# Performance work log

Hardware: AMD Instinct MI355X
Metric: run time of the kernel (lower is better)

Reference implementation:

```python
import jax, jax.numpy as jnp
import numpy as np

NODE_FEAT_DIM = 140
CONFIG_FEAT_DIM = 24
N_OPS = 120
OP_EMB_DIM = 8
H_DIM = 64
N_LAYERS = 3
N_NODES = 5000
N_EDGES = 8000
N_CONFIGS = 32
IN_DIM = NODE_FEAT_DIM + OP_EMB_DIM + CONFIG_FEAT_DIM  # 172


def setup_inputs() -> dict:
    key = jax.random.key(0)
    ks = jax.random.split(key, 24)
    s = 0.05
    inp = {
        'node_feat': jax.random.normal(ks[0], (1, N_NODES, NODE_FEAT_DIM), jnp.float32),
        'node_opcode': jax.random.randint(ks[1], (1, N_NODES), 0, N_OPS, jnp.int64),
        'edge_index': jax.random.randint(ks[2], (1, N_EDGES, 2), 0, N_NODES, jnp.int64),
        'config_feat': jax.random.normal(ks[3], (1, N_CONFIGS, CONFIG_FEAT_DIM), jnp.float32),
        'op_emb': jax.random.normal(ks[4], (N_OPS, OP_EMB_DIM), jnp.float32) * s,
        # layer 0 SAGE weights (in_dim=172), layers 1..2 stacked (h->h)
        'w_self0': jax.random.normal(ks[5], (IN_DIM, H_DIM), jnp.float32) * s,
        'w_neigh0': jax.random.normal(ks[6], (IN_DIM, H_DIM), jnp.float32) * s,
        'b0': jnp.zeros((H_DIM,), jnp.float32),
        'w_self': jax.random.normal(ks[7], (N_LAYERS - 1, H_DIM, H_DIM), jnp.float32) * s,
        'w_neigh': jax.random.normal(ks[8], (N_LAYERS - 1, H_DIM, H_DIM), jnp.float32) * s,
        'b': jnp.zeros((N_LAYERS - 1, H_DIM), jnp.float32),
        'skip_w': jax.random.normal(ks[9], (N_LAYERS, H_DIM, H_DIM), jnp.float32) * s,
        'skip_b': jnp.zeros((N_LAYERS, H_DIM), jnp.float32),
        'p1_w': jax.random.normal(ks[10], (N_LAYERS * H_DIM, (N_LAYERS - 1) * H_DIM), jnp.float32) * s,
        'p1_b': jnp.zeros(((N_LAYERS - 1) * H_DIM,), jnp.float32),
        'p2_w': jax.random.normal(ks[11], ((N_LAYERS - 1) * H_DIM, H_DIM), jnp.float32) * s,
        'p2_b': jnp.zeros((H_DIM,), jnp.float32),
        'p3_w': jax.random.normal(ks[12], (H_DIM, 1), jnp.float32) * s,
        'p3_b': jnp.zeros((1,), jnp.float32),
    }
    return inp


def _sage(x, src, dst, w_self, w_neigh, bias):
    # x: (N, C, D); bidirectional mean aggregation over edges, then linear + ReLU
    n = x.shape[0]
    msg = jax.ops.segment_sum(x[src], dst, num_segments=n)          # (N, C, D)
    deg = jax.ops.segment_sum(jnp.ones(src.shape, x.dtype), dst, num_segments=n)
    agg = msg / jnp.maximum(deg, 1.0)[:, None, None]
    return jax.nn.relu(jnp.einsum('ncd,dh->nch', x, w_self)
                       + jnp.einsum('ncd,dh->nch', agg, w_neigh) + bias)


def reference(node_feat, node_opcode, edge_index, config_feat,
              op_emb, w_self0, w_neigh0, b0, w_self, w_neigh, b,
              skip_w, skip_b, p1_w, p1_b, p2_w, p2_b, p3_w, p3_b):
    nf = node_feat[0]                     # (N, 140)
    op = node_opcode[0]                   # (N,)
    ei = edge_index[0]                    # (M, 2)
    cf = config_feat[0]                   # (C, 24)
    n_nodes, n_configs = nf.shape[0], cf.shape[0]

    # early join: node feats + op embedding broadcast with config feats
    xn = jnp.concatenate([nf, op_emb[op]], axis=-1)                     # (N, 148)
    x = jnp.concatenate([
        jnp.broadcast_to(xn[:, None, :], (n_nodes, n_configs, xn.shape[-1])),
        jnp.broadcast_to(cf[None, :, :], (n_nodes, n_configs, cf.shape[-1])),
    ], axis=-1)                                                          # (N, C, 172)

    # bidirectional edge list
    src = jnp.concatenate([ei[:, 0], ei[:, 1]])
    dst = jnp.concatenate([ei[:, 1], ei[:, 0]])

    skips = []
    x = _sage(x, src, dst, w_self0, w_neigh0, b0)
    skips.append(jax.nn.relu(jnp.einsum('nch,hk->nck', x, skip_w[0]) + skip_b[0]))
    for l in range(N_LAYERS - 1):
        x = _sage(x, src, dst, w_self[l], w_neigh[l], b[l])
        skips.append(jax.nn.relu(jnp.einsum('nch,hk->nck', x, skip_w[l + 1]) + skip_b[l + 1]))

    x = jnp.concatenate(skips, axis=-1)          # (N, C, 3*H)
    x = x.sum(axis=0)                            # global_add_pool over nodes -> (C, 3*H)
    x = jax.nn.relu(x @ p1_w + p1_b)
    x = jax.nn.relu(x @ p2_w + p2_b)
    return (x @ p3_w + p3_b)[:, 0]               # (C,)
```

## Files before the change

### kernel.cpp

```cpp
#include <hip/hip_runtime.h>

#define N_NODESC 5000
#define N_EDGESC 8000
#define NCFG 32
#define HDIM 64
#define NF_DIM 140
#define OPE_DIM 8
#define XN_DIM 148
#define CF_DIM 24
#define NBLK_SAGE 512
#define NW_SAGE (NBLK_SAGE * 4)
#define NBLK_H0 512
#define NW_H0 (NBLK_H0 * 4)

using f32x4 = __attribute__((ext_vector_type(4))) float;
using bf16x8 = __attribute__((ext_vector_type(8))) short;

__device__ __forceinline__ ushort f2b(float f) {
    uint u = __float_as_uint(f);
    u += 0x7FFF + ((u >> 16) & 1);
    return (ushort)(u >> 16);
}
__device__ __forceinline__ float b2f(ushort u) {
    return __uint_as_float(((uint)u) << 16);
}

__global__ void k_deg(const int* __restrict__ ei, int* __restrict__ deg) {
    int t = blockIdx.x * blockDim.x + threadIdx.x;
    if (t >= 2 * N_EDGESC) return;
    int d;
    if (t < N_EDGESC) d = ei[2 * t + 1];
    else d = ei[2 * (t - N_EDGESC)];
    atomicAdd(&deg[d], 1);
}

__global__ void k_scan(const int* __restrict__ deg, int* __restrict__ row_ptr) {
    __shared__ int ssum[1024];
    int t = threadIdx.x;
    const int per = (N_NODESC + 1023) / 1024;
    int vals[8];
    int loc = 0;
    for (int i = 0; i < per; ++i) {
        int idx = t * per + i;
        int v = (idx < N_NODESC) ? deg[idx] : 0;
        vals[i] = loc;
        loc += v;
    }
    ssum[t] = loc;
    __syncthreads();
    for (int s = 1; s < 1024; s <<= 1) {
        int v = (t >= s) ? ssum[t - s] : 0;
        __syncthreads();
        ssum[t] += v;
        __syncthreads();
    }
    int excl = ssum[t] - loc;
    for (int i = 0; i < per; ++i) {
        int idx = t * per + i;
        if (idx < N_NODESC) row_ptr[idx] = excl + vals[i];
    }
    if (t == 1023) row_ptr[N_NODESC] = ssum[1023];
}

__global__ void k_fill(const int* __restrict__ ei, const int* __restrict__ row_ptr,
                       int* __restrict__ fill, int* __restrict__ col) {
    int t = blockIdx.x * blockDim.x + threadIdx.x;
    if (t >= 2 * N_EDGESC) return;
    int s, d;
    if (t < N_EDGESC) { s = ei[2 * t]; d = ei[2 * t + 1]; }
    else { int e = t - N_EDGESC; s = ei[2 * e + 1]; d = ei[2 * e]; }
    int pos = atomicAdd(&fill[d], 1);
    col[row_ptr[d] + pos] = s;
}

__global__ __launch_bounds__(512) void k_pack(const float* __restrict__ skw,
                                              const float* __restrict__ wsl,
                                              const float* __restrict__ wnl,
                                              ushort* __restrict__ frag) {
    int m = blockIdx.x;
    const float* W;
    switch (m) {
        case 0: W = skw; break;
        case 1: W = wsl; break;
        case 2: W = wnl; break;
        case 3: W = skw + 4096; break;
        case 4: W = wsl + 4096; break;
        case 5: W = wnl + 4096; break;
        default: W = skw + 8192; break;
    }
    int t = threadIdx.x;
    int ktnt = t >> 6, lane = t & 63;
    int kt = ktnt >> 2, nt = ktnt & 3;
    int g = lane >> 4, row16 = lane & 15;
    bf16x8 v;
#pragma unroll
    for (int j = 0; j < 8; ++j)
        v[j] = (short)f2b(W[(kt * 32 + g * 8 + j) * HDIM + nt * 16 + row16]);
    *reinterpret_cast<bf16x8*>(frag + (size_t)m * 4096 + (size_t)t * 8) = v;
}

__global__ void k_xn(const float* __restrict__ nf, const int* __restrict__ opcode,
                     const float* __restrict__ op_emb, float* __restrict__ xn) {
    int t = blockIdx.x * blockDim.x + threadIdx.x;
    if (t >= N_NODESC * XN_DIM) return;
    int n = t / XN_DIM, f = t - n * XN_DIM;
    float v;
    if (f < NF_DIM) v = nf[n * NF_DIM + f];
    else v = op_emb[opcode[n] * OPE_DIM + (f - NF_DIM)];
    xn[t] = v;
}

__global__ void k_aggn(const float* __restrict__ xn, const int* __restrict__ row_ptr,
                       const int* __restrict__ col, float* __restrict__ aggn) {
    int t = blockIdx.x * blockDim.x + threadIdx.x;
    if (t >= N_NODESC * XN_DIM) return;
    int n = t / XN_DIM, f = t - n * XN_DIM;
    int rs = row_ptr[n], re = row_ptr[n + 1];
    float s = 0.f;
    for (int j = rs; j < re; ++j) s += xn[col[j] * XN_DIM + f];
    float inv = (re > rs) ? 1.0f / (float)(re - rs) : 0.f;
    aggn[t] = s * inv;
}

__global__ void k_En(const float* __restrict__ xn, const float* __restrict__ aggn,
                     const float* __restrict__ Ws0, const float* __restrict__ Wn0,
                     float* __restrict__ En) {
    int t = blockIdx.x * blockDim.x + threadIdx.x;
    if (t >= N_NODESC * HDIM) return;
    int n = t >> 6, k = t & 63;
    const float* x = xn + n * XN_DIM;
    const float* a = aggn + n * XN_DIM;
    float s = 0.f;
    for (int d = 0; d < XN_DIM; ++d)
        s += x[d] * Ws0[d * HDIM + k] + a[d] * Wn0[d * HDIM + k];
    En[t] = s;
}

__global__ void k_cf(const float* __restrict__ cf, const float* __restrict__ Ws0,
                     const float* __restrict__ Wn0, const float* __restrict__ b0,
                     float* __restrict__ Fc, float* __restrict__ Gc) {
    int t = threadIdx.x;
    for (int i = t; i < NCFG * HDIM; i += 256) {
        int c = i >> 6, k = i & 63;
        float f = b0[k], g = 0.f;
        for (int d = 0; d < CF_DIM; ++d) {
            float v = cf[c * CF_DIM + d];
            f += v * Ws0[(XN_DIM + d) * HDIM + k];
            g += v * Wn0[(XN_DIM + d) * HDIM + k];
        }
        Fc[i] = f;
        Gc[i] = g;
    }
}

__global__ __launch_bounds__(256) void k_h0skip(
    const float* __restrict__ En, const float* __restrict__ Fc,
    const float* __restrict__ Gc, const int* __restrict__ deg,
    const ushort* __restrict__ fragSk, const float* __restrict__ skB,
    ushort* __restrict__ h0, float* __restrict__ partials) {
    __shared__ float sred[4][NCFG * HDIM];
    int lane = threadIdx.x & 63;
    int row16 = lane & 15, g = lane >> 4;
    int w = threadIdx.x >> 6;
    int gw = (blockIdx.x * 256 + threadIdx.x) >> 6;

    bf16x8 bSk[2][4];
#pragma unroll
    for (int kt = 0; kt < 2; ++kt)
#pragma unroll
        for (int nt = 0; nt < 4; ++nt)
            bSk[kt][nt] = *reinterpret_cast<const bf16x8*>(
                fragSk + ((kt * 4 + nt) * 64 + lane) * 8);
    float sb[4];
#pragma unroll
    for (int nt = 0; nt < 4; ++nt) sb[nt] = skB[nt * 16 + row16];

    float fcv[2][2][8], gcv[2][2][8];
#pragma unroll
    for (int mt = 0; mt < 2; ++mt)
#pragma unroll
        for (int kt = 0; kt < 2; ++kt) {
            int base = (row16 + 16 * mt) * HDIM + kt * 32 + g * 8;
            float4 f0 = *(const float4*)&Fc[base];
            float4 f1 = *(const float4*)&Fc[base + 4];
            float4 g0 = *(const float4*)&Gc[base];
            float4 g1 = *(const float4*)&Gc[base + 4];
            fcv[mt][kt][0] = f0.x; fcv[mt][kt][1] = f0.y; fcv[mt][kt][2] = f0.z; fcv[mt][kt][3] = f0.w;
            fcv[mt][kt][4] = f1.x; fcv[mt][kt][5] = f1.y; fcv[mt][kt][6] = f1.z; fcv[mt][kt][7] = f1.w;
            gcv[mt][kt][0] = g0.x; gcv[mt][kt][1] = g0.y; gcv[mt][kt][2] = g0.z; gcv[mt][kt][3] = g0.w;
            gcv[mt][kt][4] = g1.x; gcv[mt][kt][5] = g1.y; gcv[mt][kt][6] = g1.z; gcv[mt][kt][7] = g1.w;
        }

    f32x4 skipAcc[2][4];
#pragma unroll
    for (int mt = 0; mt < 2; ++mt)
#pragma unroll
        for (int nt = 0; nt < 4; ++nt) skipAcc[mt][nt] = f32x4{0.f, 0.f, 0.f, 0.f};

    for (int n = gw; n < N_NODESC; n += NW_H0) {
        float sc = (deg[n] > 0) ? 1.f : 0.f;
        const float* enp = En + (size_t)n * HDIM;
        float en[2][8];
#pragma unroll
        for (int kt = 0; kt < 2; ++kt) {
            float4 e0 = *(const float4*)&enp[kt * 32 + g * 8];
            float4 e1 = *(const float4*)&enp[kt * 32 + g * 8 + 4];
            en[kt][0] = e0.x; en[kt][1] = e0.y; en[kt][2] = e0.z; en[kt][3] = e0.w;
            en[kt][4] = e1.x; en[kt][5] = e1.y; en[kt][6] = e1.z; en[kt][7] = e1.w;
        }
        bf16x8 aH[2][2];
#pragma unroll
        for (int mt = 0; mt < 2; ++mt)
#pragma unroll
            for (int kt = 0; kt < 2; ++kt) {
                bf16x8 a;
#pragma unroll
                for (int j = 0; j < 8; ++j) {
                    float hv = fmaxf(en[kt][j] + fcv[mt][kt][j] + sc * gcv[mt][kt][j], 0.f);
                    a[j] = (short)f2b(hv);
                }
                aH[mt][kt] = a;
                *reinterpret_cast<bf16x8*>(
                    h0 + (size_t)n * (NCFG * HDIM) + (row16 + 16 * mt) * HDIM + kt * 32 + g * 8) = a;
            }
#pragma unroll
        for (int mt = 0; mt < 2; ++mt)
#pragma unroll
            for (int nt = 0; nt < 4; ++nt) {
                f32x4 c2 = f32x4{0.f, 0.f, 0.f, 0.f};
#pragma unroll
                for (int kt = 0; kt < 2; ++kt)
                    c2 = __builtin_amdgcn_mfma_f32_16x16x32_bf16(aH[mt][kt], bSk[kt][nt], c2, 0, 0, 0);
#pragma unroll
                for (int r = 0; r < 4; ++r)
                    skipAcc[mt][nt][r] += fmaxf(c2[r] + sb[nt], 0.f);
            }
    }

#pragma unroll
    for (int mt = 0; mt < 2; ++mt)
#pragma unroll
        for (int nt = 0; nt < 4; ++nt)
#pragma unroll
            for (int r = 0; r < 4; ++r)
                sred[w][(16 * mt + 4 * g + r) * HDIM + 16 * nt + row16] = skipAcc[mt][nt][r];
    __syncthreads();
    float* pb = partials + (size_t)blockIdx.x * (NCFG * HDIM);
#pragma unroll
    for (int q = 0; q < 2; ++q) {
        int p = threadIdx.x * 8 + q * 4;
        f32x4 s = *(const f32x4*)&sred[0][p];
        s += *(const f32x4*)&sred[1][p];
        s += *(const f32x4*)&sred[2][p];
        s += *(const f32x4*)&sred[3][p];
        *(f32x4*)&pb[p] = s;
    }
}

template <int STORE_H>
__global__ __launch_bounds__(256) void k_sage_mfma(
    const ushort* __restrict__ h_in, ushort* __restrict__ h_out,
    const ushort* __restrict__ fragWs, const ushort* __restrict__ fragWn,
    const ushort* __restrict__ fragSk,
    const float* __restrict__ bias, const float* __restrict__ skB,
    const int* __restrict__ row_ptr, const int* __restrict__ col,
    float* __restrict__ partials) {
    __shared__ ushort sstage[4][32 * 72];
    __shared__ float sred[4][NCFG * HDIM];
    int lane = threadIdx.x & 63;
    int row16 = lane & 15, g = lane >> 4;
    int w = threadIdx.x >> 6;
    int gw = (blockIdx.x * 256 + threadIdx.x) >> 6;
    ushort* st = sstage[w];

    bf16x8 bWs[2][4], bWn[2][4], bSk[2][4];
#pragma unroll
    for (int kt = 0; kt < 2; ++kt)
#pragma unroll
        for (int nt = 0; nt < 4; ++nt) {
            int fo = ((kt * 4 + nt) * 64 + lane) * 8;
            bWs[kt][nt] = *reinterpret_cast<const bf16x8*>(fragWs + fo);
            bWn[kt][nt] = *reinterpret_cast<const bf16x8*>(fragWn + fo);
            bSk[kt][nt] = *reinterpret_cast<const bf16x8*>(fragSk + fo);
        }
    float bb[4], sb[4];
#pragma unroll
    for (int nt = 0; nt < 4; ++nt) {
        bb[nt] = bias[nt * 16 + row16];
        sb[nt] = skB[nt * 16 + row16];
    }
    f32x4 skipAcc[2][4];
#pragma unroll
    for (int mt = 0; mt < 2; ++mt)
#pragma unroll
        for (int nt = 0; nt < 4; ++nt) skipAcc[mt][nt] = f32x4{0.f, 0.f, 0.f, 0.f};

    int loff[2][2];
#pragma unroll
    for (int mt = 0; mt < 2; ++mt)
#pragma unroll
        for (int kt = 0; kt < 2; ++kt)
            loff[mt][kt] = (row16 + 16 * mt) * HDIM + kt * 32 + g * 8;

    for (int n = gw; n < N_NODESC; n += NW_SAGE) {
        const ushort* hb = h_in + (size_t)n * (NCFG * HDIM);
        bf16x8 aS[2][2];
#pragma unroll
        for (int mt = 0; mt < 2; ++mt)
#pragma unroll
            for (int kt = 0; kt < 2; ++kt)
                aS[mt][kt] = *reinterpret_cast<const bf16x8*>(hb + loff[mt][kt]);

        float agg[2][2][8];
#pragma unroll
        for (int mt = 0; mt < 2; ++mt)
#pragma unroll
            for (int kt = 0; kt < 2; ++kt)
#pragma unroll
                for (int j = 0; j < 8; ++j) agg[mt][kt][j] = 0.f;
        int rs = row_ptr[n], re = row_ptr[n + 1];
        for (int e = rs; e < re; ++e) {
            const ushort* nb = h_in + (size_t)col[e] * (NCFG * HDIM);
#pragma unroll
            for (int mt = 0; mt < 2; ++mt)
#pragma unroll
                for (int kt = 0; kt < 2; ++kt) {
                    bf16x8 u = *reinterpret_cast<const bf16x8*>(nb + loff[mt][kt]);
#pragma unroll
                    for (int j = 0; j < 8; ++j) agg[mt][kt][j] += b2f((ushort)u[j]);
                }
        }
        float inv = (re > rs) ? 1.f / (float)(re - rs) : 0.f;
        bf16x8 aA[2][2];
#pragma unroll
        for (int mt = 0; mt < 2; ++mt)
#pragma unroll
            for (int kt = 0; kt < 2; ++kt)
#pragma unroll
                for (int j = 0; j < 8; ++j)
                    aA[mt][kt][j] = (short)f2b(agg[mt][kt][j] * inv);

        f32x4 C[2][4];
#pragma unroll
        for (int mt = 0; mt < 2; ++mt)
#pragma unroll
            for (int nt = 0; nt < 4; ++nt) {
                f32x4 c = f32x4{0.f, 0.f, 0.f, 0.f};
#pragma unroll
                for (int kt = 0; kt < 2; ++kt) {
                    c = __builtin_amdgcn_mfma_f32_16x16x32_bf16(aS[mt][kt], bWs[kt][nt], c, 0, 0, 0);
                    c = __builtin_amdgcn_mfma_f32_16x16x32_bf16(aA[mt][kt], bWn[kt][nt], c, 0, 0, 0);
                }
                C[mt][nt] = c;
            }

#pragma unroll
        for (int mt = 0; mt < 2; ++mt)
#pragma unroll
            for (int nt = 0; nt < 4; ++nt)
#pragma unroll
                for (int r = 0; r < 4; ++r) {
                    float hv = fmaxf(C[mt][nt][r] + bb[nt], 0.f);
                    st[(16 * mt + 4 * g + r) * 72 + 16 * nt + row16] = f2b(hv);
                }
        asm volatile("s_waitcnt lgkmcnt(0)" ::: "memory");

        if (STORE_H) {
#pragma unroll
            for (int i = 0; i < 4; ++i) {
                int e2 = i * 512 + lane * 8;
                int cc = e2 >> 6, dd = e2 & 63;
                bf16x8 v = *reinterpret_cast<const bf16x8*>(st + cc * 72 + dd);
                *reinterpret_cast<bf16x8*>(h_out + (size_t)n * (NCFG * HDIM) + e2) = v;
            }
        }

        bf16x8 aH[2][2];
#pragma unroll
        for (int mt = 0; mt < 2; ++mt)
#pragma unroll
            for (int kt = 0; kt < 2; ++kt)
                aH[mt][kt] = *reinterpret_cast<const bf16x8*>(
                    st + (row16 + 16 * mt) * 72 + kt * 32 + g * 8);
#pragma unroll
        for (int mt = 0; mt < 2; ++mt)
#pragma unroll
            for (int nt = 0; nt < 4; ++nt) {
                f32x4 c2 = f32x4{0.f, 0.f, 0.f, 0.f};
#pragma unroll
                for (int kt = 0; kt < 2; ++kt)
                    c2 = __builtin_amdgcn_mfma_f32_16x16x32_bf16(aH[mt][kt], bSk[kt][nt], c2, 0, 0, 0);
#pragma unroll
                for (int r = 0; r < 4; ++r)
                    skipAcc[mt][nt][r] += fmaxf(c2[r] + sb[nt], 0.f);
            }
        asm volatile("s_waitcnt lgkmcnt(0)" ::: "memory");
    }

#pragma unroll
    for (int mt = 0; mt < 2; ++mt)
#pragma unroll
        for (int nt = 0; nt < 4; ++nt)
#pragma unroll
            for (int r = 0; r < 4; ++r)
                sred[w][(16 * mt + 4 * g + r) * HDIM + 16 * nt + row16] = skipAcc[mt][nt][r];
    __syncthreads();
    float* pb = partials + (size_t)blockIdx.x * (NCFG * HDIM);
#pragma unroll
    for (int q = 0; q < 2; ++q) {
        int p = threadIdx.x * 8 + q * 4;
        f32x4 s = *(const f32x4*)&sred[0][p];
        s += *(const f32x4*)&sred[1][p];
        s += *(const f32x4*)&sred[2][p];
        s += *(const f32x4*)&sred[3][p];
        *(f32x4*)&pb[p] = s;
    }
}

__global__ __launch_bounds__(256) void k_redA(const float* __restrict__ partials,
                                              int nrows, float* __restrict__ part2) {
    int i = blockIdx.x * 256 + threadIdx.x;
    int jb = blockIdx.y;
    int seg = nrows >> 5;
    const float* p = partials + (size_t)jb * seg * (NCFG * HDIM) + i;
    float s = 0.f;
    for (int b = 0; b < seg; ++b) s += p[(size_t)b * (NCFG * HDIM)];
    part2[jb * (NCFG * HDIM) + i] = s;
}

__global__ __launch_bounds__(256) void k_redB(const float* __restrict__ part2,
                                              float* __restrict__ S, int lcol) {
    int i = blockIdx.x * 256 + threadIdx.x;
    float s = 0.f;
#pragma unroll
    for (int b = 0; b < 32; ++b) s += part2[b * (NCFG * HDIM) + i];
    int c = i >> 6, k = i & 63;
    S[c * (3 * HDIM) + lcol * HDIM + k] = s;
}

__global__ void k_mlp(const float* __restrict__ S,
                      const float* __restrict__ p1w, const float* __restrict__ p1b,
                      const float* __restrict__ p2w, const float* __restrict__ p2b,
                      const float* __restrict__ p3w, const float* __restrict__ p3b,
                      float* __restrict__ out) {
    int c = blockIdx.x;
    int t = threadIdx.x;
    __shared__ float sx[192];
    __shared__ float h1[128];
    __shared__ float h2[64];
    if (t < 192) sx[t] = S[c * 192 + t];
    __syncthreads();
    if (t < 128) {
        float s = p1b[t];
        for (int d = 0; d < 192; ++d) s += sx[d] * p1w[d * 128 + t];
        h1[t] = fmaxf(s, 0.f);
    }
    __syncthreads();
    if (t < 64) {
        float s = p2b[t];
        for (int d = 0; d < 128; ++d) s += h1[d] * p2w[d * 64 + t];
        h2[t] = fmaxf(s, 0.f);
    }
    __syncthreads();
    if (t == 0) {
        float s = p3b[0];
        for (int d = 0; d < 64; ++d) s += h2[d] * p3w[d];
        out[c] = s;
    }
}

extern "C" void kernel_launch(void* const* d_in, const int* in_sizes, int n_in,
                              void* d_out, int out_size, void* d_ws, size_t ws_size,
                              hipStream_t stream) {
    const float* nf  = (const float*)d_in[0];
    const int*   opc = (const int*)d_in[1];
    const int*   ei  = (const int*)d_in[2];
    const float* cf  = (const float*)d_in[3];
    const float* ope = (const float*)d_in[4];
    const float* ws0 = (const float*)d_in[5];
    const float* wn0 = (const float*)d_in[6];
    const float* b0  = (const float*)d_in[7];
    const float* wsl = (const float*)d_in[8];
    const float* wnl = (const float*)d_in[9];
    const float* bl  = (const float*)d_in[10];
    const float* skw = (const float*)d_in[11];
    const float* skb = (const float*)d_in[12];
    const float* p1w = (const float*)d_in[13];
    const float* p1b = (const float*)d_in[14];
    const float* p2w = (const float*)d_in[15];
    const float* p2b = (const float*)d_in[16];
    const float* p3w = (const float*)d_in[17];
    const float* p3b = (const float*)d_in[18];
    float* out = (float*)d_out;

    char* w = (char*)d_ws;
    auto alloc = [&](size_t bytes) {
        char* p = w;
        w += (bytes + 255) & ~(size_t)255;
        return p;
    };
    int* deg      = (int*)alloc(N_NODESC * 4);
    int* row_ptr  = (int*)alloc((N_NODESC + 1) * 4);
    int* fill     = (int*)alloc(N_NODESC * 4);
    int* col      = (int*)alloc(2 * N_EDGESC * 4);
    float* xn     = (float*)alloc((size_t)N_NODESC * XN_DIM * 4);
    float* aggn   = (float*)alloc((size_t)N_NODESC * XN_DIM * 4);
    float* En     = (float*)alloc((size_t)N_NODESC * HDIM * 4);
    float* Fc     = (float*)alloc(NCFG * HDIM * 4);
    float* Gc     = (float*)alloc(NCFG * HDIM * 4);
    float* S      = (float*)alloc(NCFG * 3 * HDIM * 4);
    float* part2  = (float*)alloc(32 * NCFG * HDIM * 4);
    ushort* frag  = (ushort*)alloc(7 * 4096 * 2);
    float* p0     = (float*)alloc((size_t)NBLK_H0 * NCFG * HDIM * 4);
    float* p1     = (float*)alloc((size_t)NBLK_SAGE * NCFG * HDIM * 4);
    float* p2     = (float*)alloc((size_t)NBLK_SAGE * NCFG * HDIM * 4);
    ushort* h0    = (ushort*)alloc((size_t)N_NODESC * NCFG * HDIM * 2);
    ushort* h1    = (ushort*)alloc((size_t)N_NODESC * NCFG * HDIM * 2);

    hipMemsetAsync(deg, 0, N_NODESC * 4, stream);
    hipMemsetAsync(fill, 0, N_NODESC * 4, stream);
    k_deg<<<(2 * N_EDGESC + 255) / 256, 256, 0, stream>>>(ei, deg);
    k_scan<<<1, 1024, 0, stream>>>(deg, row_ptr);
    k_fill<<<(2 * N_EDGESC + 255) / 256, 256, 0, stream>>>(ei, row_ptr, fill, col);
    k_pack<<<7, 512, 0, stream>>>(skw, wsl, wnl, frag);
    k_xn<<<(N_NODESC * XN_DIM + 255) / 256, 256, 0, stream>>>(nf, opc, ope, xn);
    k_aggn<<<(N_NODESC * XN_DIM + 255) / 256, 256, 0, stream>>>(xn, row_ptr, col, aggn);
    k_En<<<(N_NODESC * HDIM + 255) / 256, 256, 0, stream>>>(xn, aggn, ws0, wn0, En);
    k_cf<<<1, 256, 0, stream>>>(cf, ws0, wn0, b0, Fc, Gc);

    k_h0skip<<<NBLK_H0, 256, 0, stream>>>(En, Fc, Gc, deg, frag, skb, h0, p0);
    k_sage_mfma<1><<<NBLK_SAGE, 256, 0, stream>>>(
        h0, h1, frag + 1 * 4096, frag + 2 * 4096, frag + 3 * 4096,
        bl, skb + 64, row_ptr, col, p1);
    k_sage_mfma<0><<<NBLK_SAGE, 256, 0, stream>>>(
        h1, (ushort*)nullptr, frag + 4 * 4096, frag + 5 * 4096, frag + 6 * 4096,
        bl + 64, skb + 2 * 64, row_ptr, col, p2);

    dim3 gA(8, 32);
    k_redA<<<gA, 256, 0, stream>>>(p0, NBLK_H0, part2);
    k_redB<<<8, 256, 0, stream>>>(part2, S, 0);
    k_redA<<<gA, 256, 0, stream>>>(p1, NBLK_SAGE, part2);
    k_redB<<<8, 256, 0, stream>>>(part2, S, 1);
    k_redA<<<gA, 256, 0, stream>>>(p2, NBLK_SAGE, part2);
    k_redB<<<8, 256, 0, stream>>>(part2, S, 2);
    k_mlp<<<NCFG, 256, 0, stream>>>(S, p1w, p1b, p2w, p2b, p3w, p3b, out);
}
```

Measured before the change: 177.9 us.

## Project layer-0 features before aggregation, one node per wave, fewer kernel launches

Layer 0 now multiplies node features by both weight matrices first and aggregates the 64-wide projected neighbour values, instead of aggregating the 148-wide inputs. This cuts aggregation traffic and removes the xn and aggn buffers. The SAGE and h0 kernels switch from a grid-stride loop to one node per wave on 1250 blocks. The per-layer reductions are merged into a single 3D launch with the final stage folded into the MLP, and the config projection is folded into the pack kernel. The partial-sum buffers grow, so the reduction reads more data, and shared memory is aliased between staging and reduction, which needs an extra barrier.

```diff
diff --git a/kernel.cpp b/kernel.cpp
--- a/kernel.cpp
+++ b/kernel.cpp
@@ -8,10 +8,7 @@
 #define OPE_DIM 8
 #define XN_DIM 148
 #define CF_DIM 24
-#define NBLK_SAGE 512
-#define NW_SAGE (NBLK_SAGE * 4)
-#define NBLK_H0 512
-#define NW_H0 (NBLK_H0 * 4)
+#define NBLK 1250
 
 using f32x4 = __attribute__((ext_vector_type(4))) float;
 using bf16x8 = __attribute__((ext_vector_type(8))) short;
@@ -76,8 +73,29 @@
 __global__ __launch_bounds__(512) void k_pack(const float* __restrict__ skw,
                                               const float* __restrict__ wsl,
                                               const float* __restrict__ wnl,
-                                              ushort* __restrict__ frag) {
+                                              const float* __restrict__ cf,
+                                              const float* __restrict__ Ws0,
+                                              const float* __restrict__ Wn0,
+                                              const float* __restrict__ b0,
+                                              ushort* __restrict__ frag,
+                                              float* __restrict__ Fc,
+                                              float* __restrict__ Gc) {
     int m = blockIdx.x;
+    int t = threadIdx.x;
+    if (m == 7) {
+        for (int i = t; i < NCFG * HDIM; i += 512) {
+            int c = i >> 6, k = i & 63;
+            float f = b0[k], g = 0.f;
+            for (int d = 0; d < CF_DIM; ++d) {
+                float v = cf[c * CF_DIM + d];
+                f += v * Ws0[(XN_DIM + d) * HDIM + k];
+                g += v * Wn0[(XN_DIM + d) * HDIM + k];
+            }
+            Fc[i] = f;
+            Gc[i] = g;
+        }
+        return;
+    }
     const float* W;
     switch (m) {
         case 0: W = skw; break;
@@ -88,7 +106,6 @@
         case 5: W = wnl + 4096; break;
         default: W = skw + 8192; break;
     }
-    int t = threadIdx.x;
     int ktnt = t >> 6, lane = t & 63;
     int kt = ktnt >> 2, nt = ktnt & 3;
     int g = lane >> 4, row16 = lane & 15;
@@ -99,70 +116,53 @@
     *reinterpret_cast<bf16x8*>(frag + (size_t)m * 4096 + (size_t)t * 8) = v;
 }
 
-__global__ void k_xn(const float* __restrict__ nf, const int* __restrict__ opcode,
-                     const float* __restrict__ op_emb, float* __restrict__ xn) {
-    int t = blockIdx.x * blockDim.x + threadIdx.x;
-    if (t >= N_NODESC * XN_DIM) return;
-    int n = t / XN_DIM, f = t - n * XN_DIM;
-    float v;
-    if (f < NF_DIM) v = nf[n * NF_DIM + f];
-    else v = op_emb[opcode[n] * OPE_DIM + (f - NF_DIM)];
-    xn[t] = v;
-}
-
-__global__ void k_aggn(const float* __restrict__ xn, const int* __restrict__ row_ptr,
-                       const int* __restrict__ col, float* __restrict__ aggn) {
-    int t = blockIdx.x * blockDim.x + threadIdx.x;
-    if (t >= N_NODESC * XN_DIM) return;
-    int n = t / XN_DIM, f = t - n * XN_DIM;
-    int rs = row_ptr[n], re = row_ptr[n + 1];
-    float s = 0.f;
-    for (int j = rs; j < re; ++j) s += xn[col[j] * XN_DIM + f];
-    float inv = (re > rs) ? 1.0f / (float)(re - rs) : 0.f;
-    aggn[t] = s * inv;
-}
-
-__global__ void k_En(const float* __restrict__ xn, const float* __restrict__ aggn,
-                     const float* __restrict__ Ws0, const float* __restrict__ Wn0,
-                     float* __restrict__ En) {
+__global__ void k_proj(const float* __restrict__ nf, const int* __restrict__ opcode,
+                       const float* __restrict__ op_emb,
+                       const float* __restrict__ Ws0, const float* __restrict__ Wn0,
+                       float* __restrict__ xs, float* __restrict__ yn) {
     int t = blockIdx.x * blockDim.x + threadIdx.x;
     if (t >= N_NODESC * HDIM) return;
     int n = t >> 6, k = t & 63;
-    const float* x = xn + n * XN_DIM;
-    const float* a = aggn + n * XN_DIM;
+    const float* x = nf + (size_t)n * NF_DIM;
+    float s = 0.f, y = 0.f;
+    for (int d = 0; d < NF_DIM; ++d) {
+        float v = x[d];
+        s += v * Ws0[d * HDIM + k];
+        y += v * Wn0[d * HDIM + k];
+    }
+    const float* oe = op_emb + (size_t)opcode[n] * OPE_DIM;
+    for (int d = 0; d < OPE_DIM; ++d) {
+        float v = oe[d];
+        s += v * Ws0[(NF_DIM + d) * HDIM + k];
+        y += v * Wn0[(NF_DIM + d) * HDIM + k];
+    }
+    xs[t] = s;
+    yn[t] = y;
+}
+
+__global__ void k_En2(const float* __restrict__ xs, const float* __restrict__ yn,
+                      const int* __restrict__ row_ptr, const int* __restrict__ col,
+                      float* __restrict__ En) {
+    int t = blockIdx.x * blockDim.x + threadIdx.x;
+    if (t >= N_NODESC * HDIM) return;
+    int n = t >> 6, k = t & 63;
+    int rs = row_ptr[n], re = row_ptr[n + 1];
     float s = 0.f;
-    for (int d = 0; d < XN_DIM; ++d)
-        s += x[d] * Ws0[d * HDIM + k] + a[d] * Wn0[d * HDIM + k];
-    En[t] = s;
-}
-
-__global__ void k_cf(const float* __restrict__ cf, const float* __restrict__ Ws0,
-                     const float* __restrict__ Wn0, const float* __restrict__ b0,
-                     float* __restrict__ Fc, float* __restrict__ Gc) {
-    int t = threadIdx.x;
-    for (int i = t; i < NCFG * HDIM; i += 256) {
-        int c = i >> 6, k = i & 63;
-        float f = b0[k], g = 0.f;
-        for (int d = 0; d < CF_DIM; ++d) {
-            float v = cf[c * CF_DIM + d];
-            f += v * Ws0[(XN_DIM + d) * HDIM + k];
-            g += v * Wn0[(XN_DIM + d) * HDIM + k];
-        }
-        Fc[i] = f;
-        Gc[i] = g;
-    }
+    for (int j = rs; j < re; ++j) s += yn[col[j] * HDIM + k];
+    float inv = (re > rs) ? 1.f / (float)(re - rs) : 0.f;
+    En[t] = xs[t] + s * inv;
 }
 
 __global__ __launch_bounds__(256) void k_h0skip(
     const float* __restrict__ En, const float* __restrict__ Fc,
-    const float* __restrict__ Gc, const int* __restrict__ deg,
+    const float* __restrict__ Gc, const int* __restrict__ row_ptr,
     const ushort* __restrict__ fragSk, const float* __restrict__ skB,
     ushort* __restrict__ h0, float* __restrict__ partials) {
     __shared__ float sred[4][NCFG * HDIM];
     int lane = threadIdx.x & 63;
     int row16 = lane & 15, g = lane >> 4;
     int w = threadIdx.x >> 6;
-    int gw = (blockIdx.x * 256 + threadIdx.x) >> 6;
+    int n = (blockIdx.x * 256 + threadIdx.x) >> 6;
 
     bf16x8 bSk[2][4];
 #pragma unroll
@@ -191,51 +191,44 @@
             gcv[mt][kt][4] = g1.x; gcv[mt][kt][5] = g1.y; gcv[mt][kt][6] = g1.z; gcv[mt][kt][7] = g1.w;
         }
 
+    float sc = (row_ptr[n + 1] > row_ptr[n]) ? 1.f : 0.f;
+    const float* enp = En + (size_t)n * HDIM;
+    float en[2][8];
+#pragma unroll
+    for (int kt = 0; kt < 2; ++kt) {
+        float4 e0 = *(const float4*)&enp[kt * 32 + g * 8];
+        float4 e1 = *(const float4*)&enp[kt * 32 + g * 8 + 4];
+        en[kt][0] = e0.x; en[kt][1] = e0.y; en[kt][2] = e0.z; en[kt][3] = e0.w;
+        en[kt][4] = e1.x; en[kt][5] = e1.y; en[kt][6] = e1.z; en[kt][7] = e1.w;
+    }
+    bf16x8 aH[2][2];
+#pragma unroll
+    for (int mt = 0; mt < 2; ++mt)
+#pragma unroll
+        for (int kt = 0; kt < 2; ++kt) {
+            bf16x8 a;
+#pragma unroll
+            for (int j = 0; j < 8; ++j) {
+                float hv = fmaxf(en[kt][j] + fcv[mt][kt][j] + sc * gcv[mt][kt][j], 0.f);
+                a[j] = (short)f2b(hv);
+            }
+            aH[mt][kt] = a;
+            *reinterpret_cast<bf16x8*>(
+                h0 + (size_t)n * (NCFG * HDIM) + (row16 + 16 * mt) * HDIM + kt * 32 + g * 8) = a;
+        }
     f32x4 skipAcc[2][4];
 #pragma unroll
     for (int mt = 0; mt < 2; ++mt)
 #pragma unroll
-        for (int nt = 0; nt < 4; ++nt) skipAcc[mt][nt] = f32x4{0.f, 0.f, 0.f, 0.f};
-
-    for (int n = gw; n < N_NODESC; n += NW_H0) {
-        float sc = (deg[n] > 0) ? 1.f : 0.f;
-        const float* enp = En + (size_t)n * HDIM;
-        float en[2][8];
-#pragma unroll
-        for (int kt = 0; kt < 2; ++kt) {
-            float4 e0 = *(const float4*)&enp[kt * 32 + g * 8];
-            float4 e1 = *(const float4*)&enp[kt * 32 + g * 8 + 4];
-            en[kt][0] = e0.x; en[kt][1] = e0.y; en[kt][2] = e0.z; en[kt][3] = e0.w;
-            en[kt][4] = e1.x; en[kt][5] = e1.y; en[kt][6] = e1.z; en[kt][7] = e1.w;
-        }
-        bf16x8 aH[2][2];
-#pragma unroll
-        for (int mt = 0; mt < 2; ++mt)
-#pragma unroll
-            for (int kt = 0; kt < 2; ++kt) {
-                bf16x8 a;
-#pragma unroll
-                for (int j = 0; j < 8; ++j) {
-                    float hv = fmaxf(en[kt][j] + fcv[mt][kt][j] + sc * gcv[mt][kt][j], 0.f);
-                    a[j] = (short)f2b(hv);
-                }
-                aH[mt][kt] = a;
-                *reinterpret_cast<bf16x8*>(
-                    h0 + (size_t)n * (NCFG * HDIM) + (row16 + 16 * mt) * HDIM + kt * 32 + g * 8) = a;
-            }
-#pragma unroll
-        for (int mt = 0; mt < 2; ++mt)
-#pragma unroll
-            for (int nt = 0; nt < 4; ++nt) {
-                f32x4 c2 = f32x4{0.f, 0.f, 0.f, 0.f};
-#pragma unroll
-                for (int kt = 0; kt < 2; ++kt)
-                    c2 = __builtin_amdgcn_mfma_f32_16x16x32_bf16(aH[mt][kt], bSk[kt][nt], c2, 0, 0, 0);
-#pragma unroll
-                for (int r = 0; r < 4; ++r)
-                    skipAcc[mt][nt][r] += fmaxf(c2[r] + sb[nt], 0.f);
-            }
-    }
+        for (int nt = 0; nt < 4; ++nt) {
+            f32x4 c2 = f32x4{0.f, 0.f, 0.f, 0.f};
+#pragma unroll
+            for (int kt = 0; kt < 2; ++kt)
+                c2 = __builtin_amdgcn_mfma_f32_16x16x32_bf16(aH[mt][kt], bSk[kt][nt], c2, 0, 0, 0);
+#pragma unroll
+            for (int r = 0; r < 4; ++r)
+                skipAcc[mt][nt][r] = fmaxf(c2[r] + sb[nt], 0.f);
+        }
 
 #pragma unroll
     for (int mt = 0; mt < 2; ++mt)
@@ -265,13 +258,13 @@
     const float* __restrict__ bias, const float* __restrict__ skB,
     const int* __restrict__ row_ptr, const int* __restrict__ col,
     float* __restrict__ partials) {
-    __shared__ ushort sstage[4][32 * 72];
-    __shared__ float sred[4][NCFG * HDIM];
+    __shared__ __align__(16) char smem_raw[NCFG * HDIM * 4 * 4];
     int lane = threadIdx.x & 63;
     int row16 = lane & 15, g = lane >> 4;
     int w = threadIdx.x >> 6;
-    int gw = (blockIdx.x * 256 + threadIdx.x) >> 6;
-    ushort* st = sstage[w];
+    int n = (blockIdx.x * 256 + threadIdx.x) >> 6;
+    ushort* st = (ushort*)smem_raw + (size_t)w * (32 * 72);
+    float* sredw = (float*)smem_raw;
 
     bf16x8 bWs[2][4], bWn[2][4], bSk[2][4];
 #pragma unroll
@@ -289,11 +282,6 @@
         bb[nt] = bias[nt * 16 + row16];
         sb[nt] = skB[nt * 16 + row16];
     }
-    f32x4 skipAcc[2][4];
-#pragma unroll
-    for (int mt = 0; mt < 2; ++mt)
-#pragma unroll
-        for (int nt = 0; nt < 4; ++nt) skipAcc[mt][nt] = f32x4{0.f, 0.f, 0.f, 0.f};
 
     int loff[2][2];
 #pragma unroll
@@ -302,143 +290,138 @@
         for (int kt = 0; kt < 2; ++kt)
             loff[mt][kt] = (row16 + 16 * mt) * HDIM + kt * 32 + g * 8;
 
-    for (int n = gw; n < N_NODESC; n += NW_SAGE) {
-        const ushort* hb = h_in + (size_t)n * (NCFG * HDIM);
-        bf16x8 aS[2][2];
+    const ushort* hb = h_in + (size_t)n * (NCFG * HDIM);
+    bf16x8 aS[2][2];
+#pragma unroll
+    for (int mt = 0; mt < 2; ++mt)
+#pragma unroll
+        for (int kt = 0; kt < 2; ++kt)
+            aS[mt][kt] = *reinterpret_cast<const bf16x8*>(hb + loff[mt][kt]);
+
+    float agg[2][2][8];
+#pragma unroll
+    for (int mt = 0; mt < 2; ++mt)
+#pragma unroll
+        for (int kt = 0; kt < 2; ++kt)
+#pragma unroll
+            for (int j = 0; j < 8; ++j) agg[mt][kt][j] = 0.f;
+    int rs = row_ptr[n], re = row_ptr[n + 1];
+    for (int e = rs; e < re; ++e) {
+        const ushort* nb = h_in + (size_t)col[e] * (NCFG * HDIM);
 #pragma unroll
         for (int mt = 0; mt < 2; ++mt)
 #pragma unroll
+            for (int kt = 0; kt < 2; ++kt) {
+                bf16x8 u = *reinterpret_cast<const bf16x8*>(nb + loff[mt][kt]);
+#pragma unroll
+                for (int j = 0; j < 8; ++j) agg[mt][kt][j] += b2f((ushort)u[j]);
+            }
+    }
+    float inv = (re > rs) ? 1.f / (float)(re - rs) : 0.f;
+    bf16x8 aA[2][2];
+#pragma unroll
+    for (int mt = 0; mt < 2; ++mt)
+#pragma unroll
+        for (int kt = 0; kt < 2; ++kt)
+#pragma unroll
+            for (int j = 0; j < 8; ++j)
+                aA[mt][kt][j] = (short)f2b(agg[mt][kt][j] * inv);
+
+    f32x4 C[2][4];
+#pragma unroll
+    for (int mt = 0; mt < 2; ++mt)
+#pragma unroll
+        for (int nt = 0; nt < 4; ++nt) {
+            f32x4 c = f32x4{0.f, 0.f, 0.f, 0.f};
+#pragma unroll
+            for (int kt = 0; kt < 2; ++kt) {
+                c = __builtin_amdgcn_mfma_f32_16x16x32_bf16(aS[mt][kt], bWs[kt][nt], c, 0, 0, 0);
+                c = __builtin_amdgcn_mfma_f32_16x16x32_bf16(aA[mt][kt], bWn[kt][nt], c, 0, 0, 0);
+            }
+            C[mt][nt] = c;
+        }
+
+#pragma unroll
+    for (int mt = 0; mt < 2; ++mt)
+#pragma unroll
+        for (int nt = 0; nt < 4; ++nt)
+#pragma unroll
+            for (int r = 0; r < 4; ++r) {
+                float hv = fmaxf(C[mt][nt][r] + bb[nt], 0.f);
+                st[(16 * mt + 4 * g + r) * 72 + 16 * nt + row16] = f2b(hv);
+            }
+    asm volatile("s_waitcnt lgkmcnt(0)" ::: "memory");
+
+    if (STORE_H) {
+#pragma unroll
+        for (int i = 0; i < 4; ++i) {
+            int e2 = i * 512 + lane * 8;
+            int cc = e2 >> 6, dd = e2 & 63;
+            bf16x8 v = *reinterpret_cast<const bf16x8*>(st + cc * 72 + dd);
+            *reinterpret_cast<bf16x8*>(h_out + (size_t)n * (NCFG * HDIM) + e2) = v;
+        }
+    }
+
+    bf16x8 aH[2][2];
+#pragma unroll
+    for (int mt = 0; mt < 2; ++mt)
+#pragma unroll
+        for (int kt = 0; kt < 2; ++kt)
+            aH[mt][kt] = *reinterpret_cast<const bf16x8*>(
+                st + (row16 + 16 * mt) * 72 + kt * 32 + g * 8);
+    asm volatile("s_waitcnt lgkmcnt(0)" ::: "memory");
+    f32x4 skipAcc[2][4];
+#pragma unroll
+    for (int mt = 0; mt < 2; ++mt)
+#pragma unroll
+        for (int nt = 0; nt < 4; ++nt) {
+            f32x4 c2 = f32x4{0.f, 0.f, 0.f, 0.f};
+#pragma unroll
             for (int kt = 0; kt < 2; ++kt)
-                aS[mt][kt] = *reinterpret_cast<const bf16x8*>(hb + loff[mt][kt]);
-
-        float agg[2][2][8];
-#pragma unroll
-        for (int mt = 0; mt < 2; ++mt)
-#pragma unroll
-            for (int kt = 0; kt < 2; ++kt)
-#pragma unroll
-                for (int j = 0; j < 8; ++j) agg[mt][kt][j] = 0.f;
-        int rs = row_ptr[n], re = row_ptr[n + 1];
-        for (int e = rs; e < re; ++e) {
-            const ushort* nb = h_in + (size_t)col[e] * (NCFG * HDIM);
-#pragma unroll
-            for (int mt = 0; mt < 2; ++mt)
-#pragma unroll
-                for (int kt = 0; kt < 2; ++kt) {
-                    bf16x8 u = *reinterpret_cast<const bf16x8*>(nb + loff[mt][kt]);
-#pragma unroll
-                    for (int j = 0; j < 8; ++j) agg[mt][kt][j] += b2f((ushort)u[j]);
-                }
-        }
-        float inv = (re > rs) ? 1.f / (float)(re - rs) : 0.f;
-        bf16x8 aA[2][2];
-#pragma unroll
-        for (int mt = 0; mt < 2; ++mt)
-#pragma unroll
-            for (int kt = 0; kt < 2; ++kt)
-#pragma unroll
-                for (int j = 0; j < 8; ++j)
-                    aA[mt][kt][j] = (short)f2b(agg[mt][kt][j] * inv);
-
-        f32x4 C[2][4];
-#pragma unroll
-        for (int mt = 0; mt < 2; ++mt)
-#pragma unroll
-            for (int nt = 0; nt < 4; ++nt) {
-                f32x4 c = f32x4{0.f, 0.f, 0.f, 0.f};
-#pragma unroll
-                for (int kt = 0; kt < 2; ++kt) {
-                    c = __builtin_amdgcn_mfma_f32_16x16x32_bf16(aS[mt][kt], bWs[kt][nt], c, 0, 0, 0);
-                    c = __builtin_amdgcn_mfma_f32_16x16x32_bf16(aA[mt][kt], bWn[kt][nt], c, 0, 0, 0);
-                }
-                C[mt][nt] = c;
-            }
-
-#pragma unroll
-        for (int mt = 0; mt < 2; ++mt)
-#pragma unroll
-            for (int nt = 0; nt < 4; ++nt)
-#pragma unroll
-                for (int r = 0; r < 4; ++r) {
-                    float hv = fmaxf(C[mt][nt][r] + bb[nt], 0.f);
-                    st[(16 * mt + 4 * g + r) * 72 + 16 * nt + row16] = f2b(hv);
-                }
-        asm volatile("s_waitcnt lgkmcnt(0)" ::: "memory");
-
-        if (STORE_H) {
-#pragma unroll
-            for (int i = 0; i < 4; ++i) {
-                int e2 = i * 512 + lane * 8;
-                int cc = e2 >> 6, dd = e2 & 63;
-                bf16x8 v = *reinterpret_cast<const bf16x8*>(st + cc * 72 + dd);
-                *reinterpret_cast<bf16x8*>(h_out + (size_t)n * (NCFG * HDIM) + e2) = v;
-            }
-        }
-
-        bf16x8 aH[2][2];
-#pragma unroll
-        for (int mt = 0; mt < 2; ++mt)
-#pragma unroll
-            for (int kt = 0; kt < 2; ++kt)
-                aH[mt][kt] = *reinterpret_cast<const bf16x8*>(
-                    st + (row16 + 16 * mt) * 72 + kt * 32 + g * 8);
-#pragma unroll
-        for (int mt = 0; mt < 2; ++mt)
-#pragma unroll
-            for (int nt = 0; nt < 4; ++nt) {
-                f32x4 c2 = f32x4{0.f, 0.f, 0.f, 0.f};
-#pragma unroll
-                for (int kt = 0; kt < 2; ++kt)
-                    c2 = __builtin_amdgcn_mfma_f32_16x16x32_bf16(aH[mt][kt], bSk[kt][nt], c2, 0, 0, 0);
-#pragma unroll
-                for (int r = 0; r < 4; ++r)
-                    skipAcc[mt][nt][r] += fmaxf(c2[r] + sb[nt], 0.f);
-            }
-        asm volatile("s_waitcnt lgkmcnt(0)" ::: "memory");
-    }
-
+                c2 = __builtin_amdgcn_mfma_f32_16x16x32_bf16(aH[mt][kt], bSk[kt][nt], c2, 0, 0, 0);
+#pragma unroll
+            for (int r = 0; r < 4; ++r)
+                skipAcc[mt][nt][r] = fmaxf(c2[r] + sb[nt], 0.f);
+        }
+
+    __syncthreads();
 #pragma unroll
     for (int mt = 0; mt < 2; ++mt)
 #pragma unroll
         for (int nt = 0; nt < 4; ++nt)
 #pragma unroll
             for (int r = 0; r < 4; ++r)
-                sred[w][(16 * mt + 4 * g + r) * HDIM + 16 * nt + row16] = skipAcc[mt][nt][r];
+                sredw[(size_t)w * (NCFG * HDIM) +
+                      (16 * mt + 4 * g + r) * HDIM + 16 * nt + row16] = skipAcc[mt][nt][r];
     __syncthreads();
     float* pb = partials + (size_t)blockIdx.x * (NCFG * HDIM);
 #pragma unroll
     for (int q = 0; q < 2; ++q) {
         int p = threadIdx.x * 8 + q * 4;
-        f32x4 s = *(const f32x4*)&sred[0][p];
-        s += *(const f32x4*)&sred[1][p];
-        s += *(const f32x4*)&sred[2][p];
-        s += *(const f32x4*)&sred[3][p];
+        f32x4 s = *(const f32x4*)&sredw[0 * NCFG * HDIM + p];
+        s += *(const f32x4*)&sredw[1 * NCFG * HDIM + p];
+        s += *(const f32x4*)&sredw[2 * NCFG * HDIM + p];
+        s += *(const f32x4*)&sredw[3 * NCFG * HDIM + p];
         *(f32x4*)&pb[p] = s;
     }
 }
 
-__global__ __launch_bounds__(256) void k_redA(const float* __restrict__ partials,
-                                              int nrows, float* __restrict__ part2) {
+__global__ __launch_bounds__(256) void k_redA(const float* __restrict__ pAll,
+                                              float* __restrict__ part2) {
     int i = blockIdx.x * 256 + threadIdx.x;
     int jb = blockIdx.y;
-    int seg = nrows >> 5;
-    const float* p = partials + (size_t)jb * seg * (NCFG * HDIM) + i;
+    int l = blockIdx.z;
+    const int seg = (NBLK + 31) / 32;
+    const float* base = pAll + (size_t)l * NBLK * (NCFG * HDIM);
     float s = 0.f;
-    for (int b = 0; b < seg; ++b) s += p[(size_t)b * (NCFG * HDIM)];
-    part2[jb * (NCFG * HDIM) + i] = s;
-}
-
-__global__ __launch_bounds__(256) void k_redB(const float* __restrict__ part2,
-                                              float* __restrict__ S, int lcol) {
-    int i = blockIdx.x * 256 + threadIdx.x;
-    float s = 0.f;
-#pragma unroll
-    for (int b = 0; b < 32; ++b) s += part2[b * (NCFG * HDIM) + i];
-    int c = i >> 6, k = i & 63;
-    S[c * (3 * HDIM) + lcol * HDIM + k] = s;
-}
-
-__global__ void k_mlp(const float* __restrict__ S,
+    for (int q = 0; q < seg; ++q) {
+        int b = jb * seg + q;
+        if (b < NBLK) s += base[(size_t)b * (NCFG * HDIM) + i];
+    }
+    part2[((size_t)l * 32 + jb) * (NCFG * HDIM) + i] = s;
+}
+
+__global__ void k_mlp(const float* __restrict__ part2,
                       const float* __restrict__ p1w, const float* __restrict__ p1b,
                       const float* __restrict__ p2w, const float* __restrict__ p2b,
                       const float* __restrict__ p3w, const float* __restrict__ p3b,
@@ -448,7 +431,14 @@
     __shared__ float sx[192];
     __shared__ float h1[128];
     __shared__ float h2[64];
-    if (t < 192) sx[t] = S[c * 192 + t];
+    if (t < 192) {
+        int l = t >> 6, k = t & 63;
+        float s = 0.f;
+#pragma unroll
+        for (int b = 0; b < 32; ++b)
+            s += part2[((size_t)l * 32 + b) * (NCFG * HDIM) + c * HDIM + k];
+        sx[t] = s;
+    }
     __syncthreads();
     if (t < 128) {
         float s = p1b[t];
@@ -500,48 +490,41 @@
         return p;
     };
     int* deg      = (int*)alloc(N_NODESC * 4);
+    int* fill     = (int*)alloc(N_NODESC * 4);
     int* row_ptr  = (int*)alloc((N_NODESC + 1) * 4);
-    int* fill     = (int*)alloc(N_NODESC * 4);
     int* col      = (int*)alloc(2 * N_EDGESC * 4);
-    float* xn     = (float*)alloc((size_t)N_NODESC * XN_DIM * 4);
-    float* aggn   = (float*)alloc((size_t)N_NODESC * XN_DIM * 4);
+    float* xs     = (float*)alloc((size_t)N_NODESC * HDIM * 4);
+    float* yn     = (float*)alloc((size_t)N_NODESC * HDIM * 4);
     float* En     = (float*)alloc((size_t)N_NODESC * HDIM * 4);
     float* Fc     = (float*)alloc(NCFG * HDIM * 4);
     float* Gc     = (float*)alloc(NCFG * HDIM * 4);
-    float* S      = (float*)alloc(NCFG * 3 * HDIM * 4);
-    float* part2  = (float*)alloc(32 * NCFG * HDIM * 4);
+    float* part2  = (float*)alloc(3 * 32 * NCFG * HDIM * 4);
     ushort* frag  = (ushort*)alloc(7 * 4096 * 2);
-    float* p0     = (float*)alloc((size_t)NBLK_H0 * NCFG * HDIM * 4);
-    float* p1     = (float*)alloc((size_t)NBLK_SAGE * NCFG * HDIM * 4);
-    float* p2     = (float*)alloc((size_t)NBLK_SAGE * NCFG * HDIM * 4);
+    float* pAll   = (float*)alloc((size_t)3 * NBLK * NCFG * HDIM * 4);
     ushort* h0    = (ushort*)alloc((size_t)N_NODESC * NCFG * HDIM * 2);
     ushort* h1    = (ushort*)alloc((size_t)N_NODESC * NCFG * HDIM * 2);
 
-    hipMemsetAsync(deg, 0, N_NODESC * 4, stream);
-    hipMemsetAsync(fill, 0, N_NODESC * 4, stream);
+    float* p0 = pAll;
+    float* p1 = pAll + (size_t)NBLK * (NCFG * HDIM);
+    float* p2 = pAll + (size_t)2 * NBLK * (NCFG * HDIM);
+
+    hipMemsetAsync(deg, 0, ((N_NODESC * 4 + 255) & ~255) * 2, stream);
     k_deg<<<(2 * N_EDGESC + 255) / 256, 256, 0, stream>>>(ei, deg);
     k_scan<<<1, 1024, 0, stream>>>(deg, row_ptr);
     k_fill<<<(2 * N_EDGESC + 255) / 256, 256, 0, stream>>>(ei, row_ptr, fill, col);
-    k_pack<<<7, 512, 0, stream>>>(skw, wsl, wnl, frag);
-    k_xn<<<(N_NODESC * XN_DIM + 255) / 256, 256, 0, stream>>>(nf, opc, ope, xn);
-    k_aggn<<<(N_NODESC * XN_DIM + 255) / 256, 256, 0, stream>>>(xn, row_ptr, col, aggn);
-    k_En<<<(N_NODESC * HDIM + 255) / 256, 256, 0, stream>>>(xn, aggn, ws0, wn0, En);
-    k_cf<<<1, 256, 0, stream>>>(cf, ws0, wn0, b0, Fc, Gc);
-
-    k_h0skip<<<NBLK_H0, 256, 0, stream>>>(En, Fc, Gc, deg, frag, skb, h0, p0);
-    k_sage_mfma<1><<<NBLK_SAGE, 256, 0, stream>>>(
+    k_pack<<<8, 512, 0, stream>>>(skw, wsl, wnl, cf, ws0, wn0, b0, frag, Fc, Gc);
+    k_proj<<<(N_NODESC * HDIM + 255) / 256, 256, 0, stream>>>(nf, opc, ope, ws0, wn0, xs, yn);
+    k_En2<<<(N_NODESC * HDIM + 255) / 256, 256, 0, stream>>>(xs, yn, row_ptr, col, En);
+
+    k_h0skip<<<NBLK, 256, 0, stream>>>(En, Fc, Gc, row_ptr, frag, skb, h0, p0);
+    k_sage_mfma<1><<<NBLK, 256, 0, stream>>>(
         h0, h1, frag + 1 * 4096, frag + 2 * 4096, frag + 3 * 4096,
         bl, skb + 64, row_ptr, col, p1);
-    k_sage_mfma<0><<<NBLK_SAGE, 256, 0, stream>>>(
+    k_sage_mfma<0><<<NBLK, 256, 0, stream>>>(
         h1, (ushort*)nullptr, frag + 4 * 4096, frag + 5 * 4096, frag + 6 * 4096,
         bl + 64, skb + 2 * 64, row_ptr, col, p2);
 
-    dim3 gA(8, 32);
-    k_redA<<<gA, 256, 0, stream>>>(p0, NBLK_H0, part2);
-    k_redB<<<8, 256, 0, stream>>>(part2, S, 0);
-    k_redA<<<gA, 256, 0, stream>>>(p1, NBLK_SAGE, part2);
-    k_redB<<<8, 256, 0, stream>>>(part2, S, 1);
-    k_redA<<<gA, 256, 0, stream>>>(p2, NBLK_SAGE, part2);
-    k_redB<<<8, 256, 0, stream>>>(part2, S, 2);
-    k_mlp<<<NCFG, 256, 0, stream>>>(S, p1w, p1b, p2w, p2b, p3w, p3b, out);
-}
+    dim3 gA(8, 32, 3);
+    k_redA<<<gA, 256, 0, stream>>>(pAll, part2);
+    k_mlp<<<NCFG, 256, 0, stream>>>(part2, p1w, p1b, p2w, p2b, p3w, p3b, out);
+}
```

After: 149.6 us. -15.9%, faster.
